# Performance work log

Hardware: AMD Instinct MI355X
Metric: run time of the kernel (lower is better)

The kernel has to match this reference:

```python
import jax, jax.numpy as jnp
import numpy as np

B, S, E, H = 1, 2048, 2048, 32
D = E // H  # head_dim = 64
QMAX = 127.0


def _ste(x, xq):
    # straight-through fake quant (forward = xq, grad = identity)
    return x + jax.lax.stop_gradient(xq - x)


def fake_quant_act(x):
    # per-tensor symmetric int8 fake quantization (QuantMatMul.quant_x*/act quantizer)
    scale = jnp.maximum(jnp.max(jnp.abs(x)) / QMAX, 1e-8)
    xq = jnp.clip(jnp.round(x / scale), -128.0, QMAX) * scale
    return _ste(x, xq)


def fake_quant_weight(w):
    # per-output-channel symmetric int8 fake quantization (weight quantizer)
    scale = jnp.maximum(jnp.max(jnp.abs(w), axis=1, keepdims=True) / QMAX, 1e-8)
    wq = jnp.clip(jnp.round(w / scale), -128.0, QMAX) * scale
    return _ste(w, wq)


def rope_cos_sin(seq_len, dim):
    inv_freq = 1.0 / (10000.0 ** (jnp.arange(0, dim, 2, dtype=jnp.float32) / dim))
    t = jnp.arange(seq_len, dtype=jnp.float32)
    freqs = jnp.outer(t, inv_freq)            # [S, D/2]
    emb = jnp.concatenate([freqs, freqs], -1)  # [S, D]
    return jnp.cos(emb), jnp.sin(emb)


def rotate_half(x):
    x1, x2 = jnp.split(x, 2, axis=-1)
    return jnp.concatenate([-x2, x1], axis=-1)


def setup_inputs() -> dict:
    key = jax.random.key(0)
    ks = jax.random.split(key, 5)
    return {
        "hidden_states": jax.random.normal(ks[0], (B, S, E), dtype=jnp.float32),
        "w_q": jax.random.normal(ks[1], (E, E), dtype=jnp.float32) * 0.02,
        "w_k": jax.random.normal(ks[2], (E, E), dtype=jnp.float32) * 0.02,
        "w_v": jax.random.normal(ks[3], (E, E), dtype=jnp.float32) * 0.02,
        "w_o": jax.random.normal(ks[4], (E, E), dtype=jnp.float32) * 0.02,
    }


def reference(hidden_states, w_q, w_k, w_v, w_o):
    scaling = D ** -0.5
    # quantized projections (QuantLinear: fake-quant weight, no input quant for q/k/v)
    q = hidden_states @ fake_quant_weight(w_q).T * scaling
    k = hidden_states @ fake_quant_weight(w_k).T
    v = hidden_states @ fake_quant_weight(w_v).T
    # qkt_matmul.quant_x1/quant_x2, pv_matmul.quant_x2
    q = fake_quant_act(q)
    k = fake_quant_act(k)
    v = fake_quant_act(v)
    # [B,S,E] -> [B,H,S,D]
    q = q.reshape(B, S, H, D).transpose(0, 2, 1, 3)
    k = k.reshape(B, S, H, D).transpose(0, 2, 1, 3)
    v = v.reshape(B, S, H, D).transpose(0, 2, 1, 3)
    # rotary embedding
    cos, sin = rope_cos_sin(S, D)
    cos = cos[None, None]
    sin = sin[None, None]
    q = q * cos + rotate_half(q) * sin
    k = k * cos + rotate_half(k) * sin
    # QK^T (already scaled via q) + causal mask
    scores = jnp.einsum("bhsd,bhtd->bhst", q, k)  # [B,H,S,S]
    causal = jnp.tril(jnp.ones((S, S), dtype=bool))
    scores = jnp.where(causal[None, None], scores, jnp.finfo(scores.dtype).min)
    probs = jax.nn.softmax(scores.astype(jnp.float32), axis=-1).astype(q.dtype)
    # PV matmul (v already fake-quantized)
    out = jnp.einsum("bhst,bhtd->bhsd", probs, v)
    out = out.transpose(0, 2, 1, 3).reshape(B, S, E)
    # o_proj: QuantLinear with input quant enabled
    out = fake_quant_act(out) @ fake_quant_weight(w_o).T
    return out
```

## Files before the change

kernel.cpp:

```cpp
#include <hip/hip_runtime.h>
#include <hip/hip_bf16.h>
#include <hip/hip_fp16.h>

#define S_LEN 2048
#define E_DIM 2048
#define H_NUM 32
#define D_DIM 64

typedef __attribute__((ext_vector_type(8))) short short8;
typedef __attribute__((ext_vector_type(4))) short short4v;
typedef __attribute__((ext_vector_type(4))) float f32x4;
typedef __attribute__((ext_vector_type(4))) int i32x4;

__device__ __forceinline__ unsigned short f2h(float f) {
  return __builtin_bit_cast(unsigned short, (_Float16)f);
}

__device__ __forceinline__ float h2f(unsigned short u) {
  return (float)__builtin_bit_cast(_Float16, u);
}

__device__ __forceinline__ float fq1(float x, float invs, float scale) {
  return fminf(fmaxf(rintf(x * invs), -128.f), 127.f) * scale;
}

__device__ __forceinline__ int q8(float x, float invs) {
  return min(max((int)rintf(x * invs), -128), 127);
}

__device__ __forceinline__ void gload_lds16(const void* g, void* l) {
  __builtin_amdgcn_global_load_lds((const __attribute__((address_space(1))) void*)g,
                                   (__attribute__((address_space(3))) void*)l, 16, 0, 0);
}

__device__ __forceinline__ f32x4 mfma16h(short8 a, short8 b, f32x4 c) {
  return __builtin_amdgcn_mfma_f32_16x16x32_f16(a, b, c, 0, 0, 0);
}

__device__ __forceinline__ i32x4 mfma16i8(i32x4 a, i32x4 b, i32x4 c) {
  return __builtin_amdgcn_mfma_i32_16x16x64_i8(a, b, c, 0, 0, 0);
}

#define VMW4() asm volatile("s_waitcnt vmcnt(4)" ::: "memory")
#define VMW3() asm volatile("s_waitcnt vmcnt(3)" ::: "memory")
#define VMW0() asm volatile("s_waitcnt vmcnt(0)" ::: "memory")
#define BARR() asm volatile("s_barrier" ::: "memory")
#define LGKM0() asm volatile("s_waitcnt lgkmcnt(0)" ::: "memory")
#define SCHB() __builtin_amdgcn_sched_barrier(0)

__global__ void k_prep(const float* __restrict__ hs,
                       const float* __restrict__ w_q, const float* __restrict__ w_k,
                       const float* __restrict__ w_v, const float* __restrict__ w_o,
                       unsigned short* __restrict__ hsb, unsigned short* __restrict__ wq_all,
                       signed char* __restrict__ wo_i8, float* __restrict__ wsc,
                       unsigned* __restrict__ sc, float2* __restrict__ trig) {
  const int b = blockIdx.x;
  if (b < 4096) {
    int i = b * 256 + threadIdx.x;
    float4 v = ((const float4*)hs)[i];
    ushort4 r;
    r.x = f2h(v.x); r.y = f2h(v.y); r.z = f2h(v.z); r.w = f2h(v.w);
    ((ushort4*)hsb)[i] = r;
    return;
  }
  if (b >= 12288) {
    if (b == 12288) {
      if (threadIdx.x < 8) sc[threadIdx.x] = 0u;
      return;
    }
    int idx = (b - 12289) * 256 + threadIdx.x;
    int s = idx >> 5, i = idx & 31;
    float freq = exp2f(-(float)i * (13.287712379549449f / 32.f));
    float ang = (float)s * freq;
    float sn, cs;
    sincosf(ang, &sn, &cs);
    float2 t; t.x = cs; t.y = sn;
    trig[idx] = t;
    return;
  }
  __shared__ float wm[4];
  const int isWo = (b >= 10240);
  const int bb = isWo ? (b - 10240) : (b - 4096);
  const int wy = isWo ? 0 : (bb >> 11);
  const int wx = isWo ? bb : (bb & 2047);
  const float* w = isWo ? w_o : (wy == 0 ? w_q : wy == 1 ? w_k : w_v);
  const float* row = w + (size_t)wx * E_DIM;
  float4 a = ((const float4*)row)[threadIdx.x * 2];
  float4 bq = ((const float4*)row)[threadIdx.x * 2 + 1];
  float m = fmaxf(fmaxf(fmaxf(fabsf(a.x), fabsf(a.y)), fmaxf(fabsf(a.z), fabsf(a.w))),
                  fmaxf(fmaxf(fabsf(bq.x), fabsf(bq.y)), fmaxf(fabsf(bq.z), fabsf(bq.w))));
#pragma unroll
  for (int off = 32; off; off >>= 1) m = fmaxf(m, __shfl_xor(m, off));
  if ((threadIdx.x & 63) == 0) wm[threadIdx.x >> 6] = m;
  __syncthreads();
  m = fmaxf(fmaxf(wm[0], wm[1]), fmaxf(wm[2], wm[3]));
  float scale = fmaxf(m * (1.f / 127.f), 1e-8f);
  float invs = 1.f / scale;
  if (isWo) {
    unsigned lo = (unsigned)(q8(a.x, invs) & 255) | ((unsigned)(q8(a.y, invs) & 255) << 8) |
                  ((unsigned)(q8(a.z, invs) & 255) << 16) | ((unsigned)(q8(a.w, invs) & 255) << 24);
    unsigned hi = (unsigned)(q8(bq.x, invs) & 255) | ((unsigned)(q8(bq.y, invs) & 255) << 8) |
                  ((unsigned)(q8(bq.z, invs) & 255) << 16) | ((unsigned)(q8(bq.w, invs) & 255) << 24);
    uint2 pk; pk.x = lo; pk.y = hi;
    ((uint2*)(wo_i8 + (size_t)wx * E_DIM))[threadIdx.x] = pk;
    if (threadIdx.x == 0) wsc[wx] = scale;
  } else {
    unsigned short* orow = wq_all + (size_t)wy * E_DIM * E_DIM + (size_t)wx * E_DIM;
    ushort4 r0, r1;
    r0.x = f2h(fq1(a.x, invs, scale)); r0.y = f2h(fq1(a.y, invs, scale));
    r0.z = f2h(fq1(a.z, invs, scale)); r0.w = f2h(fq1(a.w, invs, scale));
    r1.x = f2h(fq1(bq.x, invs, scale)); r1.y = f2h(fq1(bq.y, invs, scale));
    r1.z = f2h(fq1(bq.z, invs, scale)); r1.w = f2h(fq1(bq.w, invs, scale));
    ((ushort4*)orow)[threadIdx.x * 2] = r0;
    ((ushort4*)orow)[threadIdx.x * 2 + 1] = r1;
  }
}

__global__ __launch_bounds__(512, 2)
void k_gemm_qkv(const unsigned short* __restrict__ A, const unsigned short* __restrict__ Bt,
                unsigned short* __restrict__ C, unsigned* __restrict__ amax, float alpha_q) {
  __shared__ char lds[131072];
  const int K = 2048, NT = 32;
  const int lin = blockIdx.x;
  const int swz = (lin & 7) * 24 + (lin >> 3);
  const int z = swz >> 6;
  const int t64 = swz & 63;
  const int iby = t64 >> 3;
  const int ibx = t64 & 7;
  const unsigned short* Bz = Bt + (size_t)z * E_DIM * E_DIM;
  unsigned short* Cz = C + (size_t)z * S_LEN * E_DIM;
  const float alpha = (z == 0) ? alpha_q : 1.0f;

  const int tid = threadIdx.x;
  const int wv = tid >> 6, ln = tid & 63;
  const int wm = wv >> 2, wn = wv & 3;
  const size_t bm = (size_t)ibx * 256, bn = (size_t)iby * 256;
  const int arow = ln & 15, gsl = ln >> 4;

  int abyte[8], bbyte[4];
#pragma unroll
  for (int i = 0; i < 8; ++i) {
    int r = wm * 128 + i * 16 + arow;
    abyte[i] = r * 64 + ((gsl ^ ((r >> 1) & 3)) * 16);
  }
#pragma unroll
  for (int j = 0; j < 4; ++j) {
    int r = wn * 64 + j * 16 + arow;
    bbyte[j] = 32768 + r * 64 + ((gsl ^ ((r >> 1) & 3)) * 16);
  }

  const int srow = tid >> 2;
  const int scc = (tid & 3) ^ ((tid >> 3) & 3);
  const unsigned short* Asrc = A + (bm + srow) * (size_t)K + scc * 8;
  const unsigned short* Bsrc = Bz + (bn + srow) * (size_t)K + scc * 8;
  const int ldst = tid * 16;

#define STGA(T, S) do { \
    char* d_ = lds + ((T) & 1) * 65536 + (S) * 16384 + ldst; \
    const unsigned short* s_ = Asrc + (T) * 64 + (S) * 32; \
    gload_lds16(s_, d_); \
    gload_lds16(s_ + (size_t)128 * K, d_ + 8192); } while (0)
#define STGB(T, S) do { \
    char* d_ = lds + ((T) & 1) * 65536 + 32768 + (S) * 16384 + ldst; \
    const unsigned short* s_ = Bsrc + (T) * 64 + (S) * 32; \
    gload_lds16(s_, d_); \
    gload_lds16(s_ + (size_t)128 * K, d_ + 8192); } while (0)

  f32x4 acc[8][4];
#pragma unroll
  for (int i = 0; i < 8; ++i)
#pragma unroll
    for (int j = 0; j < 4; ++j) { acc[i][j][0] = 0.f; acc[i][j][1] = 0.f; acc[i][j][2] = 0.f; acc[i][j][3] = 0.f; }

  STGA(0, 0); STGB(0, 0); STGA(0, 1); STGB(0, 1);
  VMW4();
  BARR();

#define TILE(BUF, DS, T1, W2X, W4X) do { \
    char* bp_ = lds + (BUF); \
    short8 af_[4], bf_[4], ag_[4]; \
     \
    _Pragma("unroll") for (int i = 0; i < 4; ++i) af_[i] = *(const short8*)(bp_ + abyte[i]); \
    _Pragma("unroll") for (int j = 0; j < 4; ++j) bf_[j] = *(const short8*)(bp_ + bbyte[j]); \
    if (DS) STGA(T1, 0); \
    BARR(); LGKM0(); SCHB(); \
    __builtin_amdgcn_s_setprio(1); \
    _Pragma("unroll") for (int i = 0; i < 4; ++i) \
      _Pragma("unroll") for (int j = 0; j < 4; ++j) acc[i][j] = mfma16h(af_[i], bf_[j], acc[i][j]); \
    __builtin_amdgcn_s_setprio(0); \
    BARR(); \
     \
    _Pragma("unroll") for (int i = 0; i < 4; ++i) ag_[i] = *(const short8*)(bp_ + abyte[4 + i]); \
    if (DS) STGB(T1, 0); \
    BARR(); LGKM0(); SCHB(); \
    __builtin_amdgcn_s_setprio(1); \
    _Pragma("unroll") for (int i = 0; i < 4; ++i) \
      _Pragma("unroll") for (int j = 0; j < 4; ++j) acc[4 + i][j] = mfma16h(ag_[i], bf_[j], acc[4 + i][j]); \
    __builtin_amdgcn_s_setprio(0); \
    W2X; \
    BARR(); \
     \
    _Pragma("unroll") for (int i = 0; i < 4; ++i) af_[i] = *(const short8*)(bp_ + 16384 + abyte[i]); \
    _Pragma("unroll") for (int j = 0; j < 4; ++j) bf_[j] = *(const short8*)(bp_ + 16384 + bbyte[j]); \
    if (DS) STGA(T1, 1); \
    BARR(); LGKM0(); SCHB(); \
    __builtin_amdgcn_s_setprio(1); \
    _Pragma("unroll") for (int i = 0; i < 4; ++i) \
      _Pragma("unroll") for (int j = 0; j < 4; ++j) acc[i][j] = mfma16h(af_[i], bf_[j], acc[i][j]); \
    __builtin_amdgcn_s_setprio(0); \
    BARR(); \
     \
    _Pragma("unroll") for (int i = 0; i < 4; ++i) ag_[i] = *(const short8*)(bp_ + 16384 + abyte[4 + i]); \
    if (DS) STGB(T1, 1); \
    BARR(); LGKM0(); SCHB(); \
    __builtin_amdgcn_s_setprio(1); \
    _Pragma("unroll") for (int i = 0; i < 4; ++i) \
      _Pragma("unroll") for (int j = 0; j < 4; ++j) acc[4 + i][j] = mfma16h(ag_[i], bf_[j], acc[4 + i][j]); \
    __builtin_amdgcn_s_setprio(0); \
    W4X; \
    BARR(); \
  } while (0)

#pragma unroll 1
  for (int t = 0; t < NT - 2; t += 2) {
    TILE(0, 1, t + 1, VMW4(), VMW4());
    TILE(65536, 1, t + 2, VMW4(), VMW4());
  }
  TILE(0, 1, NT - 1, VMW4(), VMW4());
  TILE(65536, 0, 0, VMW0(), (void)0);
#undef TILE
#undef STGA
#undef STGB

  float amx = 0.f;
#pragma unroll
  for (int i = 0; i < 8; ++i) {
    size_t rowb = bm + wm * 128 + i * 16 + gsl * 4;
#pragma unroll
    for (int j = 0; j < 4; ++j) {
      size_t col = bn + wn * 64 + j * 16 + arow;
#pragma unroll
      for (int r = 0; r < 4; ++r) {
        float v = acc[i][j][r] * alpha;
        Cz[(rowb + r) * E_DIM + col] = f2h(v);
        amx = fmaxf(amx, fabsf(v));
      }
    }
  }
#pragma unroll
  for (int off = 32; off; off >>= 1) amx = fmaxf(amx, __shfl_xor(amx, off));
  if (ln == 0) atomicMax(amax + z, __float_as_uint(amx));
}

__global__ __launch_bounds__(256, 4)
void k_gemm_o(const signed char* __restrict__ A, const signed char* __restrict__ Bt,
              float* __restrict__ C, const unsigned* __restrict__ sc,
              const float* __restrict__ wsc) {
  __shared__ char lds[36864];
  const int K = 2048, NT = 32;
  const float sa = fmaxf(__uint_as_float(sc[3]) * (1.f / 127.f), 1e-8f);
  const int lin = blockIdx.y * 16 + blockIdx.x;
  const int swz = (lin & 7) * 64 + (lin >> 3);
  const int iby = swz >> 4;
  const int ibx = swz & 15;

  const int tid = threadIdx.x;
  const int wv = tid >> 6, ln = tid & 63;
  const int wm = wv >> 1, wn = wv & 1;
  const size_t bm = (size_t)ibx * 128, bn = (size_t)iby * 64;
  const int arow = ln & 15, gsl = ln >> 4;

  int abyte[4], bbyte[2];
#pragma unroll
  for (int i = 0; i < 4; ++i) {
    int ra = wm * 64 + i * 16 + arow;
    abyte[i] = ra * 64 + ((gsl ^ ((ra >> 1) & 3)) * 16);
  }
#pragma unroll
  for (int j = 0; j < 2; ++j) {
    int rb = wn * 32 + j * 16 + arow;
    bbyte[j] = rb * 64 + ((gsl ^ ((rb >> 1) & 3)) * 16);
  }

  const int srow = tid >> 2;
  const int sl = (tid & 3) ^ ((srow >> 1) & 3);
  const signed char* Ast = A + (bm + srow) * (size_t)K + sl * 16;
  const signed char* Bst = Bt + (bn + srow) * (size_t)K + sl * 16;

#define STG(T, dst) do { if ((T) < NT) { \
    size_t go = (size_t)(T) * 64; \
    gload_lds16(Ast + go, (dst) + wv * 1024); \
    gload_lds16(Ast + go + (size_t)64 * K, (dst) + 4096 + wv * 1024); \
    gload_lds16(Bst + go, (dst) + 8192 + wv * 1024); } } while (0)

  i32x4 acc[4][2];
#pragma unroll
  for (int i = 0; i < 4; ++i)
#pragma unroll
    for (int j = 0; j < 2; ++j) { acc[i][j][0] = 0; acc[i][j][1] = 0; acc[i][j][2] = 0; acc[i][j][3] = 0; }

  char* b0 = lds;
  char* b1 = lds + 12288;
  char* b2 = lds + 24576;

  STG(0, b0); STG(1, b1);
  VMW3();
  BARR();

#define ITER(T, bufR, bufS) do { \
    i32x4 af[4], bf[2]; \
    _Pragma("unroll") \
    for (int i = 0; i < 4; ++i) af[i] = *(const i32x4*)((bufR) + abyte[i]); \
    _Pragma("unroll") \
    for (int j = 0; j < 2; ++j) bf[j] = *(const i32x4*)((bufR) + 8192 + bbyte[j]); \
    STG((T) + 2, bufS); \
    __builtin_amdgcn_s_setprio(1); \
    _Pragma("unroll") \
    for (int i = 0; i < 4; ++i) \
      _Pragma("unroll") \
      for (int j = 0; j < 2; ++j) acc[i][j] = mfma16i8(af[i], bf[j], acc[i][j]); \
    __builtin_amdgcn_s_setprio(0); \
    if ((T) == NT - 2) { VMW0(); } else if ((T) < NT - 2) { VMW3(); } \
    BARR(); } while (0)

#pragma unroll 1
  for (int t = 0; t + 2 < NT; t += 3) {
    ITER(t, b0, b2);
    ITER(t + 1, b1, b0);
    ITER(t + 2, b2, b1);
  }
  ITER(NT - 2, b0, b2);
  ITER(NT - 1, b1, b0);
#undef ITER
#undef STG

#pragma unroll
  for (int i = 0; i < 4; ++i) {
    size_t rowb = bm + wm * 64 + i * 16 + gsl * 4;
#pragma unroll
    for (int j = 0; j < 2; ++j) {
      size_t col = bn + wn * 32 + j * 16 + arow;
      float s = sa * wsc[col];
#pragma unroll
      for (int r = 0; r < 4; ++r)
        C[(rowb + r) * E_DIM + col] = (float)acc[i][j][r] * s;
    }
  }
}

__global__ void k_rvt(const unsigned short* __restrict__ qkv,
                      unsigned short* __restrict__ Qh, unsigned short* __restrict__ Kh,
                      unsigned short* __restrict__ Vt, const unsigned* __restrict__ sc,
                      const float2* __restrict__ trig) {
  __shared__ float tb[64][65];
  const int z = blockIdx.z;
  if (z < 2) {
    const unsigned short* x = qkv + (z ? 4194304 : 0);
    unsigned short* out = z ? Kh : Qh;
    float scale = fmaxf(__uint_as_float(sc[z]) * (1.f / 127.f), 1e-8f);
    float invs = 1.f / scale;
    int h = blockIdx.y;
    int s = blockIdx.x * 8 + (threadIdx.x >> 5);
    int i = threadIdx.x & 31;
    size_t base = (size_t)s * E_DIM + h * 64 + i;
    float x0 = h2f(x[base]);
    float x1 = h2f(x[base + 32]);
    float q0 = fq1(x0, invs, scale);
    float q1 = fq1(x1, invs, scale);
    float2 t = trig[s * 32 + i];
    size_t ob = (size_t)h * S_LEN * D_DIM + (size_t)s * D_DIM + i;
    out[ob] = f2h(q0 * t.x - q1 * t.y);
    out[ob + 32] = f2h(q1 * t.x + q0 * t.y);
    return;
  }
  if (blockIdx.x >= 32) return;
  const unsigned short* v = qkv + 2 * 4194304;
  float scale = fmaxf(__uint_as_float(sc[2]) * (1.f / 127.f), 1e-8f);
  float invs = 1.f / scale;
  int s0 = blockIdx.x * 64, h = blockIdx.y;
#pragma unroll
  for (int l = 0; l < 16; ++l) {
    int idx = threadIdx.x + l * 256;
    int r = idx >> 6, c = idx & 63;
    float x = h2f(v[(size_t)(s0 + r) * E_DIM + h * 64 + c]);
    tb[r][c] = fq1(x, invs, scale);
  }
  __syncthreads();
#pragma unroll
  for (int l = 0; l < 16; ++l) {
    int idx = threadIdx.x + l * 256;
    int d = idx >> 6, s = idx & 63;
    Vt[(size_t)h * D_DIM * S_LEN + (size_t)d * S_LEN + s0 + s] = f2h(tb[s][d]);
  }
}

__global__ __launch_bounds__(256, 4)
void k_attn(const unsigned short* __restrict__ Qh, const unsigned short* __restrict__ Kh,
            const unsigned short* __restrict__ Vt, unsigned short* __restrict__ att,
            unsigned* __restrict__ amax) {
  __shared__ char Kbuf[2 * 8192];
  __shared__ char Vbuf[2 * 8192];
  __shared__ __align__(16) char Pb[8192];
  const int L = blockIdx.x;
  const int h = L & 31;
  const int qc = 31 - (L >> 5);
  const int nt = qc + 1;
  const int tid = threadIdx.x;
  const int wv = tid >> 6, ln = tid & 63;
  const int arow = ln & 15, gsl = ln >> 4;
  const unsigned short* Qb = Qh + (size_t)h * S_LEN * D_DIM;
  const unsigned short* Kb = Kh + (size_t)h * S_LEN * D_DIM;
  const unsigned short* Vb = Vt + (size_t)h * D_DIM * S_LEN;
  const int qr = qc * 64 + wv * 16;

  const int srow0 = tid >> 3, sch0 = (tid & 7) ^ (srow0 & 7);
  const int srow1 = 32 + (tid >> 3), sch1 = (tid & 7) ^ (srow1 & 7);

#define STAGEK(T, B) do { char* kd = Kbuf + (B) * 8192; const int tb_ = (T) * 64; \
    gload_lds16(Kb + (size_t)(tb_ + srow0) * D_DIM + sch0 * 8, kd + wv * 1024); \
    gload_lds16(Kb + (size_t)(tb_ + srow1) * D_DIM + sch1 * 8, kd + 4096 + wv * 1024); } while (0)
#define STAGEV(T, B) do { char* vd = Vbuf + (B) * 8192; const int tb_ = (T) * 64; \
    gload_lds16(Vb + (size_t)srow0 * S_LEN + tb_ + sch0 * 8, vd + wv * 1024); \
    gload_lds16(Vb + (size_t)srow1 * S_LEN + tb_ + sch1 * 8, vd + 4096 + wv * 1024); } while (0)

  short8 qa0 = *(const short8*)(Qb + (size_t)(qr + arow) * D_DIM + gsl * 8);
  short8 qa1 = *(const short8*)(Qb + (size_t)(qr + arow) * D_DIM + 32 + gsl * 8);

  f32x4 o[4];
  float mrow = -INFINITY, lrow = 0.f;
#pragma unroll
  for (int d = 0; d < 4; ++d) { o[d][0] = 0.f; o[d][1] = 0.f; o[d][2] = 0.f; o[d][3] = 0.f; }

  STAGEK(0, 0);
  STAGEV(0, 0);
  if (nt > 1) { STAGEK(1, 1); STAGEV(1, 1); VMW4(); } else { VMW0(); }
  BARR();

  char* Pw = Pb + wv * 2048 + arow * 128;
  const int arw7 = arow & 7;

#pragma unroll 1
  for (int t = 0; t < nt; ++t) {
    if (t >= 1 && t + 1 < nt) { STAGEK(t + 1, (t + 1) & 1); STAGEV(t + 1, (t + 1) & 1); }
    char* kb = Kbuf + (t & 1) * 8192;
    char* vb = Vbuf + (t & 1) * 8192;

    short8 kf[4][2];
#pragma unroll
    for (int kvb = 0; kvb < 4; ++kvb) {
      int row = kvb * 16 + arow;
      int sw = (row & 7) << 4;
      kf[kvb][0] = *(const short8*)(kb + row * 128 + ((gsl * 16) ^ sw));
      kf[kvb][1] = *(const short8*)(kb + row * 128 + ((64 + gsl * 16) ^ sw));
    }
    f32x4 s4[4];
#pragma unroll
    for (int kvb = 0; kvb < 4; ++kvb) {
      s4[kvb][0] = 0.f; s4[kvb][1] = 0.f; s4[kvb][2] = 0.f; s4[kvb][3] = 0.f;
    }
#pragma unroll
    for (int kvb = 0; kvb < 4; ++kvb) {
      s4[kvb] = mfma16h(kf[kvb][0], qa0, s4[kvb]);
      s4[kvb] = mfma16h(kf[kvb][1], qa1, s4[kvb]);
    }

    const int t0 = t * 64;
    const int qrow = qr + arow;
    if (t0 + 63 > qrow) {
#pragma unroll
      for (int kvb = 0; kvb < 4; ++kvb) {
        int colb = t0 + kvb * 16 + gsl * 4;
#pragma unroll
        for (int r = 0; r < 4; ++r)
          if (colb + r > qrow) s4[kvb][r] = -INFINITY;
      }
    }

    float smax = s4[0][0];
#pragma unroll
    for (int kvb = 0; kvb < 4; ++kvb)
#pragma unroll
      for (int r = 0; r < 4; ++r) smax = fmaxf(smax, s4[kvb][r]);
    smax = fmaxf(smax, __shfl_xor(smax, 16));
    smax = fmaxf(smax, __shfl_xor(smax, 32));

    float mn = fmaxf(mrow, smax);
    float corr = __expf(mrow - mn);
    mrow = mn;

    float rs = 0.f;
    float p[4][4];
#pragma unroll
    for (int kvb = 0; kvb < 4; ++kvb)
#pragma unroll
      for (int r = 0; r < 4; ++r) {
        p[kvb][r] = __expf(s4[kvb][r] - mn);
        rs += p[kvb][r];
      }
    rs += __shfl_xor(rs, 16);
    rs += __shfl_xor(rs, 32);
    lrow = lrow * corr + rs;

    float corr_r[4];
#pragma unroll
    for (int r = 0; r < 4; ++r) corr_r[r] = __shfl(corr, gsl * 4 + r);
#pragma unroll
    for (int d = 0; d < 4; ++d)
#pragma unroll
      for (int r = 0; r < 4; ++r) o[d][r] *= corr_r[r];

    __builtin_amdgcn_wave_barrier();
#pragma unroll
    for (int kvb = 0; kvb < 4; ++kvb) {
      short4v pw;
      pw[0] = (short)f2h(p[kvb][0]);
      pw[1] = (short)f2h(p[kvb][1]);
      pw[2] = (short)f2h(p[kvb][2]);
      pw[3] = (short)f2h(p[kvb][3]);
      const int u = kvb * 2 + (gsl >> 1);
      *(short4v*)(Pw + ((u ^ arw7) << 4) + ((gsl & 1) << 3)) = pw;
    }
    __builtin_amdgcn_wave_barrier();
    short8 pa0 = *(const short8*)(Pw + ((gsl ^ arw7) << 4));
    short8 pa1 = *(const short8*)(Pw + (((4 + gsl) ^ arw7) << 4));
    __builtin_amdgcn_wave_barrier();

    short8 vf[4][2];
#pragma unroll
    for (int d = 0; d < 4; ++d) {
      int row = d * 16 + arow;
      int sw = (row & 7) << 4;
      vf[d][0] = *(const short8*)(vb + row * 128 + ((gsl * 16) ^ sw));
      vf[d][1] = *(const short8*)(vb + row * 128 + ((64 + gsl * 16) ^ sw));
    }
#pragma unroll
    for (int d = 0; d < 4; ++d) {
      o[d] = mfma16h(pa0, vf[d][0], o[d]);
      o[d] = mfma16h(pa1, vf[d][1], o[d]);
    }

    VMW0();
    BARR();
  }
#undef STAGEK
#undef STAGEV

  float amx = 0.f;
  float invl = 1.f / lrow;
  float invl_r[4];
#pragma unroll
  for (int r = 0; r < 4; ++r) invl_r[r] = __shfl(invl, gsl * 4 + r);
#pragma unroll
  for (int r = 0; r < 4; ++r) {
    size_t row = (size_t)(qr + gsl * 4 + r);
#pragma unroll
    for (int d = 0; d < 4; ++d) {
      float v = o[d][r] * invl_r[r];
      att[row * E_DIM + h * 64 + d * 16 + arow] = f2h(v);
      amx = fmaxf(amx, fabsf(v));
    }
  }

#pragma unroll
  for (int off = 32; off; off >>= 1) amx = fmaxf(amx, __shfl_xor(amx, off));
  if (ln == 0) atomicMax(amax + 3, __float_as_uint(amx));
}

__global__ void k_quant_act_i8(const unsigned short* __restrict__ in, uint2* __restrict__ out,
                               const unsigned* __restrict__ sc, int idx) {
  float scale = fmaxf(__uint_as_float(sc[idx]) * (1.f / 127.f), 1e-8f);
  float invs = 1.f / scale;
  int i = blockIdx.x * blockDim.x + threadIdx.x;
  short8 v = ((const short8*)in)[i];
  unsigned lo = 0, hi = 0;
#pragma unroll
  for (int e = 0; e < 4; ++e)
    lo |= (unsigned)(q8(h2f((unsigned short)v[e]), invs) & 255) << (8 * e);
#pragma unroll
  for (int e = 0; e < 4; ++e)
    hi |= (unsigned)(q8(h2f((unsigned short)v[4 + e]), invs) & 255) << (8 * e);
  uint2 pk; pk.x = lo; pk.y = hi;
  out[i] = pk;
}

extern "C" void kernel_launch(void* const* d_in, const int* in_sizes, int n_in,
                              void* d_out, int out_size, void* d_ws, size_t ws_size,
                              hipStream_t stream) {
  const float* hs = (const float*)d_in[0];
  const float* w_q = (const float*)d_in[1];
  const float* w_k = (const float*)d_in[2];
  const float* w_v = (const float*)d_in[3];
  const float* w_o = (const float*)d_in[4];

  char* ws = (char*)d_ws;
  unsigned short* wq_all = (unsigned short*)(ws);
  signed char* wo_i8 = (signed char*)(ws + 25165824);
  float* wsc = (float*)(ws + 29360128);
  float2* trig = (float2*)(ws + 30408704);
  unsigned short* hsb = (unsigned short*)(ws + 33554432);
  unsigned short* qkv16 = (unsigned short*)(ws + 41943040);
  unsigned short* att = qkv16;
  signed char* aq_i8 = (signed char*)(ws + 67108864);
  unsigned short* Qh = (unsigned short*)(ws + 92274688);
  unsigned short* Kh = (unsigned short*)(ws + 100663296);
  unsigned short* Vt = (unsigned short*)(ws + 109051904);
  unsigned* sc = (unsigned*)(ws + 117440512);

  k_prep<<<12545, 256, 0, stream>>>(hs, w_q, w_k, w_v, w_o, hsb, wq_all, wo_i8, wsc, sc, trig);
  k_gemm_qkv<<<dim3(192), 512, 0, stream>>>(hsb, wq_all, qkv16, sc, 0.125f);
  k_rvt<<<dim3(256, 32, 3), 256, 0, stream>>>(qkv16, Qh, Kh, Vt, sc, trig);
  k_attn<<<1024, 256, 0, stream>>>(Qh, Kh, Vt, att, sc);
  k_quant_act_i8<<<2048, 256, 0, stream>>>(att, (uint2*)aq_i8, sc, 3);
  k_gemm_o<<<dim3(16, 32), 256, 0, stream>>>(aq_i8, wo_i8, (float*)d_out, sc, wsc);
}
```

Measured before the change: 187.2 us.

## Retile QKV GEMM to 256x192 tiles spanning fused N to fill 256 CUs

```diff
diff --git a/kernel.cpp b/kernel.cpp
--- a/kernel.cpp
+++ b/kernel.cpp
@@ -46,7 +46,6 @@
 #define VMW0() asm volatile("s_waitcnt vmcnt(0)" ::: "memory")
 #define BARR() asm volatile("s_barrier" ::: "memory")
 #define LGKM0() asm volatile("s_waitcnt lgkmcnt(0)" ::: "memory")
-#define SCHB() __builtin_amdgcn_sched_barrier(0)
 
 __global__ void k_prep(const float* __restrict__ hs,
                        const float* __restrict__ w_q, const float* __restrict__ w_k,
@@ -119,103 +118,99 @@
 __global__ __launch_bounds__(512, 2)
 void k_gemm_qkv(const unsigned short* __restrict__ A, const unsigned short* __restrict__ Bt,
                 unsigned short* __restrict__ C, unsigned* __restrict__ amax, float alpha_q) {
-  __shared__ char lds[131072];
+  __shared__ char lds[114688];
   const int K = 2048, NT = 32;
   const int lin = blockIdx.x;
-  const int swz = (lin & 7) * 24 + (lin >> 3);
-  const int z = swz >> 6;
-  const int t64 = swz & 63;
-  const int iby = t64 >> 3;
-  const int ibx = t64 & 7;
-  const unsigned short* Bz = Bt + (size_t)z * E_DIM * E_DIM;
-  unsigned short* Cz = C + (size_t)z * S_LEN * E_DIM;
-  const float alpha = (z == 0) ? alpha_q : 1.0f;
+  const int swz = (lin & 7) * 32 + (lin >> 3);
+  const int ibx = swz >> 5;
+  const int iby = swz & 31;
 
   const int tid = threadIdx.x;
   const int wv = tid >> 6, ln = tid & 63;
   const int wm = wv >> 2, wn = wv & 3;
-  const size_t bm = (size_t)ibx * 256, bn = (size_t)iby * 256;
+  const size_t bm = (size_t)ibx * 256, bn = (size_t)iby * 192;
   const int arow = ln & 15, gsl = ln >> 4;
 
-  int abyte[8], bbyte[4];
+  int abyte[8], bbyte[3];
 #pragma unroll
   for (int i = 0; i < 8; ++i) {
     int r = wm * 128 + i * 16 + arow;
     abyte[i] = r * 64 + ((gsl ^ ((r >> 1) & 3)) * 16);
   }
 #pragma unroll
-  for (int j = 0; j < 4; ++j) {
-    int r = wn * 64 + j * 16 + arow;
+  for (int j = 0; j < 3; ++j) {
+    int r = wn * 48 + j * 16 + arow;
     bbyte[j] = 32768 + r * 64 + ((gsl ^ ((r >> 1) & 3)) * 16);
   }
 
   const int srow = tid >> 2;
   const int scc = (tid & 3) ^ ((tid >> 3) & 3);
   const unsigned short* Asrc = A + (bm + srow) * (size_t)K + scc * 8;
-  const unsigned short* Bsrc = Bz + (bn + srow) * (size_t)K + scc * 8;
+  const unsigned short* Bsrc = Bt + (bn + srow) * (size_t)K + scc * 8;
   const int ldst = tid * 16;
 
+#define BUFOF(T) (((T) & 1) * 57344)
 #define STGA(T, S) do { \
-    char* d_ = lds + ((T) & 1) * 65536 + (S) * 16384 + ldst; \
+    char* d_ = lds + BUFOF(T) + (S) * 16384 + ldst; \
     const unsigned short* s_ = Asrc + (T) * 64 + (S) * 32; \
     gload_lds16(s_, d_); \
     gload_lds16(s_ + (size_t)128 * K, d_ + 8192); } while (0)
 #define STGB(T, S) do { \
-    char* d_ = lds + ((T) & 1) * 65536 + 32768 + (S) * 16384 + ldst; \
+    char* d_ = lds + BUFOF(T) + 32768 + (S) * 12288 + ldst; \
     const unsigned short* s_ = Bsrc + (T) * 64 + (S) * 32; \
     gload_lds16(s_, d_); \
-    gload_lds16(s_ + (size_t)128 * K, d_ + 8192); } while (0)
-
-  f32x4 acc[8][4];
+    if (tid < 256) gload_lds16(s_ + (size_t)128 * K, d_ + 8192); } while (0)
+
+  f32x4 acc[8][3];
 #pragma unroll
   for (int i = 0; i < 8; ++i)
 #pragma unroll
-    for (int j = 0; j < 4; ++j) { acc[i][j][0] = 0.f; acc[i][j][1] = 0.f; acc[i][j][2] = 0.f; acc[i][j][3] = 0.f; }
+    for (int j = 0; j < 3; ++j) { acc[i][j][0] = 0.f; acc[i][j][1] = 0.f; acc[i][j][2] = 0.f; acc[i][j][3] = 0.f; }
 
   STGA(0, 0); STGB(0, 0); STGA(0, 1); STGB(0, 1);
-  VMW4();
+  VMW0();
   BARR();
 
 #define TILE(BUF, DS, T1, W2X, W4X) do { \
     char* bp_ = lds + (BUF); \
-    short8 af_[4], bf_[4], ag_[4]; \
+    short8 af_[4], bf_[3], ag_[4]; \
      \
     _Pragma("unroll") for (int i = 0; i < 4; ++i) af_[i] = *(const short8*)(bp_ + abyte[i]); \
-    _Pragma("unroll") for (int j = 0; j < 4; ++j) bf_[j] = *(const short8*)(bp_ + bbyte[j]); \
+    _Pragma("unroll") for (int j = 0; j < 3; ++j) bf_[j] = *(const short8*)(bp_ + bbyte[j]); \
     if (DS) STGA(T1, 0); \
-    BARR(); LGKM0(); SCHB(); \
+    BARR(); LGKM0(); \
     __builtin_amdgcn_s_setprio(1); \
     _Pragma("unroll") for (int i = 0; i < 4; ++i) \
-      _Pragma("unroll") for (int j = 0; j < 4; ++j) acc[i][j] = mfma16h(af_[i], bf_[j], acc[i][j]); \
+      _Pragma("unroll") for (int j = 0; j < 3; ++j) acc[i][j] = mfma16h(af_[i], bf_[j], acc[i][j]); \
     __builtin_amdgcn_s_setprio(0); \
     BARR(); \
      \
     _Pragma("unroll") for (int i = 0; i < 4; ++i) ag_[i] = *(const short8*)(bp_ + abyte[4 + i]); \
     if (DS) STGB(T1, 0); \
-    BARR(); LGKM0(); SCHB(); \
+    BARR(); LGKM0(); \
     __builtin_amdgcn_s_setprio(1); \
     _Pragma("unroll") for (int i = 0; i < 4; ++i) \
-      _Pragma("unroll") for (int j = 0; j < 4; ++j) acc[4 + i][j] = mfma16h(ag_[i], bf_[j], acc[4 + i][j]); \
+      _Pragma("unroll") for (int j = 0; j < 3; ++j) acc[4 + i][j] = mfma16h(ag_[i], bf_[j], acc[4 + i][j]); \
     __builtin_amdgcn_s_setprio(0); \
     W2X; \
     BARR(); \
      \
     _Pragma("unroll") for (int i = 0; i < 4; ++i) af_[i] = *(const short8*)(bp_ + 16384 + abyte[i]); \
-    _Pragma("unroll") for (int j = 0; j < 4; ++j) bf_[j] = *(const short8*)(bp_ + 16384 + bbyte[j]); \
+    _Pragma("unroll") for (int j = 0; j < 3; ++j) bf_[j] = *(const short8*)(bp_ + 12288 + bbyte[j]); \
     if (DS) STGA(T1, 1); \
-    BARR(); LGKM0(); SCHB(); \
+    BARR(); LGKM0(); \
     __builtin_amdgcn_s_setprio(1); \
     _Pragma("unroll") for (int i = 0; i < 4; ++i) \
-      _Pragma("unroll") for (int j = 0; j < 4; ++j) acc[i][j] = mfma16h(af_[i], bf_[j], acc[i][j]); \
+      _Pragma("unroll") for (int j = 0; j < 3; ++j) acc[i][j] = mfma16h(af_[i], bf_[j], acc[i][j]); \
     __builtin_amdgcn_s_setprio(0); \
     BARR(); \
      \
     _Pragma("unroll") for (int i = 0; i < 4; ++i) ag_[i] = *(const short8*)(bp_ + 16384 + abyte[4 + i]); \
     if (DS) STGB(T1, 1); \
-    BARR(); LGKM0(); SCHB(); \
+    BARR(); LGKM0(); \
     __builtin_amdgcn_s_setprio(1); \
     _Pragma("unroll") for (int i = 0; i < 4; ++i) \
-      _Pragma("unroll") for (int j = 0; j < 4; ++j) acc[4 + i][j] = mfma16h(ag_[i], bf_[j], acc[4 + i][j]); \
+      _Pragma("unroll") for (int j = 0; j < 3; ++j) acc[4 + i][j] = mfma16h(ag_[i], bf_[j], acc[4 + i][j]); \
     __builtin_amdgcn_s_setprio(0); \
     W4X; \
     BARR(); \
@@ -223,33 +218,38 @@
 
 #pragma unroll 1
   for (int t = 0; t < NT - 2; t += 2) {
-    TILE(0, 1, t + 1, VMW4(), VMW4());
-    TILE(65536, 1, t + 2, VMW4(), VMW4());
-  }
-  TILE(0, 1, NT - 1, VMW4(), VMW4());
-  TILE(65536, 0, 0, VMW0(), (void)0);
+    TILE(0, 1, t + 1, VMW3(), VMW3());
+    TILE(57344, 1, t + 2, VMW3(), VMW3());
+  }
+  TILE(0, 1, NT - 1, VMW3(), VMW3());
+  TILE(57344, 0, 0, VMW0(), (void)0);
 #undef TILE
 #undef STGA
 #undef STGB
-
-  float amx = 0.f;
-#pragma unroll
-  for (int i = 0; i < 8; ++i) {
-    size_t rowb = bm + wm * 128 + i * 16 + gsl * 4;
-#pragma unroll
-    for (int j = 0; j < 4; ++j) {
-      size_t col = bn + wn * 64 + j * 16 + arow;
+#undef BUFOF
+
+#pragma unroll
+  for (int j = 0; j < 3; ++j) {
+    const int colbase = (int)bn + wn * 48 + j * 16;
+    const int zj = colbase >> 11;
+    const float alpha = (zj == 0) ? alpha_q : 1.0f;
+    unsigned short* Cz = C + (size_t)zj * S_LEN * E_DIM;
+    const int col = (colbase & 2047) + arow;
+    float amxj = 0.f;
+#pragma unroll
+    for (int i = 0; i < 8; ++i) {
+      size_t rowb = bm + wm * 128 + i * 16 + gsl * 4;
 #pragma unroll
       for (int r = 0; r < 4; ++r) {
         float v = acc[i][j][r] * alpha;
         Cz[(rowb + r) * E_DIM + col] = f2h(v);
-        amx = fmaxf(amx, fabsf(v));
+        amxj = fmaxf(amxj, fabsf(v));
       }
     }
-  }
-#pragma unroll
-  for (int off = 32; off; off >>= 1) amx = fmaxf(amx, __shfl_xor(amx, off));
-  if (ln == 0) atomicMax(amax + z, __float_as_uint(amx));
+#pragma unroll
+    for (int off = 32; off; off >>= 1) amxj = fmaxf(amxj, __shfl_xor(amxj, off));
+    if (ln == 0) atomicMax(amax + zj, __float_as_uint(amxj));
+  }
 }
 
 __global__ __launch_bounds__(256, 4)
@@ -607,7 +607,7 @@
   unsigned* sc = (unsigned*)(ws + 117440512);
 
   k_prep<<<12545, 256, 0, stream>>>(hs, w_q, w_k, w_v, w_o, hsb, wq_all, wo_i8, wsc, sc, trig);
-  k_gemm_qkv<<<dim3(192), 512, 0, stream>>>(hsb, wq_all, qkv16, sc, 0.125f);
+  k_gemm_qkv<<<dim3(256), 512, 0, stream>>>(hsb, wq_all, qkv16, sc, 0.125f);
   k_rvt<<<dim3(256, 32, 3), 256, 0, stream>>>(qkv16, Qh, Kh, Vt, sc, trig);
   k_attn<<<1024, 256, 0, stream>>>(Qh, Kh, Vt, att, sc);
   k_quant_act_i8<<<2048, 256, 0, stream>>>(att, (uint2*)aq_i8, sc, 3);
```

New measurement: 240.2 us. +28.3%, slower.
